# Kernel tuning notes

Measured on AMD Instinct MI355X. Metric: run time of the kernel, lower is better.

The kernel has to match this reference:

```python
import jax, jax.numpy as jnp
import numpy as np

N = 50000          # nodes
E_RAND = 800000    # random edges (avg degree 16)
IN, HID, HEADS, OUT = 256, 64, 4, 40
NEG_SLOPE = 0.2    # PyG GATConv default leaky_relu slope
BN_EPS = 1e-5


def setup_inputs() -> dict:
    key = jax.random.key(0)
    ks = jax.random.split(key, 24)
    x = jax.random.normal(ks[0], (N, IN), jnp.float32)
    ei = jax.random.randint(ks[1], (2, E_RAND), 0, N)
    loops = jnp.arange(N, dtype=ei.dtype)
    edge_index = jnp.concatenate([ei, jnp.stack([loops, loops])], axis=1)  # add self loops (PyG default)
    s = 0.1
    d = {
        "x": x,
        "edge_index": edge_index,
        "W0": jax.random.normal(ks[2], (IN, HEADS * HID), jnp.float32) * s,
        "a_src0": jax.random.normal(ks[3], (HEADS, HID), jnp.float32) * s,
        "a_dst0": jax.random.normal(ks[4], (HEADS, HID), jnp.float32) * s,
        "b0": jax.random.normal(ks[5], (HEADS * HID,), jnp.float32) * s,
        "bn0_g": jnp.ones((HEADS * HID,), jnp.float32),
        "bn0_b": jnp.zeros((HEADS * HID,), jnp.float32),
        "bn0_m": jax.random.normal(ks[6], (HEADS * HID,), jnp.float32) * s,
        "bn0_v": jax.random.uniform(ks[7], (HEADS * HID,), jnp.float32, 0.5, 1.5),
        "W1": jax.random.normal(ks[8], (HEADS * HID, HEADS * HID), jnp.float32) * s,
        "a_src1": jax.random.normal(ks[9], (HEADS, HID), jnp.float32) * s,
        "a_dst1": jax.random.normal(ks[10], (HEADS, HID), jnp.float32) * s,
        "b1": jax.random.normal(ks[11], (HEADS * HID,), jnp.float32) * s,
        "bn1_g": jnp.ones((HEADS * HID,), jnp.float32),
        "bn1_b": jnp.zeros((HEADS * HID,), jnp.float32),
        "bn1_m": jax.random.normal(ks[12], (HEADS * HID,), jnp.float32) * s,
        "bn1_v": jax.random.uniform(ks[13], (HEADS * HID,), jnp.float32, 0.5, 1.5),
        "W2": jax.random.normal(ks[14], (HEADS * HID, OUT), jnp.float32) * s,
        "a_src2": jax.random.normal(ks[15], (1, OUT), jnp.float32) * s,
        "a_dst2": jax.random.normal(ks[16], (1, OUT), jnp.float32) * s,
        "b2": jax.random.normal(ks[17], (OUT,), jnp.float32) * s,
    }
    return d


def gat_conv(x, edge_index, W, att_src, att_dst, heads, ch):
    """PyG GATConv (eval mode): gather -> leaky_relu attn -> segment softmax -> scatter add."""
    src, dst = edge_index[0], edge_index[1]
    h = (x @ W).reshape(-1, heads, ch)                       # [N,H,C]
    a_s = jnp.einsum('nhc,hc->nh', h, att_src)
    a_d = jnp.einsum('nhc,hc->nh', h, att_dst)
    e = jax.nn.leaky_relu(a_s[src] + a_d[dst], NEG_SLOPE)    # [E,H]
    m = jax.ops.segment_max(e, dst, num_segments=N)
    m = jax.lax.stop_gradient(jnp.where(jnp.isfinite(m), m, 0.0))
    p = jnp.exp(e - m[dst])
    denom = jax.ops.segment_sum(p, dst, num_segments=N)
    alpha = p / (denom[dst] + 1e-16)                         # [E,H]
    msg = h[src] * alpha[:, :, None]                         # [E,H,C]
    return jax.ops.segment_sum(msg, dst, num_segments=N)     # [N,H,C]


def _bn(h, g, b, m, v):
    return g * (h - m) * jax.lax.rsqrt(v + BN_EPS) + b


def reference(x, edge_index, W0, a_src0, a_dst0, b0, bn0_g, bn0_b, bn0_m, bn0_v,
              W1, a_src1, a_dst1, b1, bn1_g, bn1_b, bn1_m, bn1_v,
              W2, a_src2, a_dst2, b2):
    h = gat_conv(x, edge_index, W0, a_src0, a_dst0, HEADS, HID).reshape(N, HEADS * HID) + b0
    h = jax.nn.elu(_bn(h, bn0_g, bn0_b, bn0_m, bn0_v))
    h = gat_conv(h, edge_index, W1, a_src1, a_dst1, HEADS, HID).reshape(N, HEADS * HID) + b1
    h = jax.nn.elu(_bn(h, bn1_g, bn1_b, bn1_m, bn1_v))
    out = gat_conv(h, edge_index, W2, a_src2, a_dst2, 1, OUT).reshape(N, OUT) + b2
    return out
```

## Files before the change

### kernel.cpp

```cpp
#include <hip/hip_runtime.h>
#include <cstdint>
#include <cstddef>

constexpr int kN = 50000;
constexpr float kSlope = 0.2f;
constexpr float kBnEps = 1e-5f;

static inline int ceil_div(int a, int b) { return (a + b - 1) / b; }

typedef __attribute__((ext_vector_type(8))) _Float16 half8;
typedef __attribute__((ext_vector_type(8))) unsigned short ushortx8;
typedef __attribute__((ext_vector_type(4))) float f32x4;

__device__ inline unsigned short f2h_us(float f) {
  _Float16 h = (_Float16)f;
  return *(unsigned short*)&h;
}

__device__ inline void gload16(const void* g, void* l) {
  __builtin_amdgcn_global_load_lds((const __attribute__((address_space(1))) unsigned int*)g,
                                   (__attribute__((address_space(3))) unsigned int*)l, 16, 0, 0);
}


__global__ void k_degree(const int* __restrict__ dst, int* __restrict__ deg, int E) {
  int e = blockIdx.x * blockDim.x + threadIdx.x;
  if (e < E) atomicAdd(&deg[dst[e]], 1);
}

__global__ void k_scan1(const int* __restrict__ deg, int* __restrict__ rp,
                        int* __restrict__ bsum, int n) {
  __shared__ int sm[256];
  int i = blockIdx.x * 256 + threadIdx.x;
  int v = (i < n) ? deg[i] : 0;
  sm[threadIdx.x] = v;
  __syncthreads();
  for (int off = 1; off < 256; off <<= 1) {
    int t = (threadIdx.x >= off) ? sm[threadIdx.x - off] : 0;
    __syncthreads();
    sm[threadIdx.x] += t;
    __syncthreads();
  }
  if (i < n) rp[i + 1] = sm[threadIdx.x];
  if (threadIdx.x == 255) bsum[blockIdx.x] = sm[255];
}

__global__ void k_scan2(int* bsum, int nb) {
  __shared__ int sm[256];
  int v = (threadIdx.x < nb) ? bsum[threadIdx.x] : 0;
  sm[threadIdx.x] = v;
  __syncthreads();
  for (int off = 1; off < 256; off <<= 1) {
    int t = (threadIdx.x >= off) ? sm[threadIdx.x - off] : 0;
    __syncthreads();
    sm[threadIdx.x] += t;
    __syncthreads();
  }
  if (threadIdx.x < nb) bsum[threadIdx.x] = sm[threadIdx.x] - v;
}

__global__ void k_scan3(int* __restrict__ rp, const int* __restrict__ bsum, int n) {
  int i = blockIdx.x * 256 + threadIdx.x;
  if (i < n) rp[i + 1] += bsum[blockIdx.x];
  if (i == 0) rp[0] = 0;
}

__global__ void k_scatter(const int* __restrict__ src, const int* __restrict__ dst,
                          const int* __restrict__ rp, int* __restrict__ cur,
                          int* __restrict__ csr, int E) {
  int e = blockIdx.x * blockDim.x + threadIdx.x;
  if (e < E) {
    int d = dst[e];
    int pos = rp[d] + atomicAdd(&cur[d], 1);
    csr[pos] = src[e];
  }
}


__global__ void k_prep(const float* __restrict__ x, unsigned short* __restrict__ x16,
                       const float* __restrict__ W0, unsigned short* __restrict__ Wt0,
                       const float* __restrict__ W1, unsigned short* __restrict__ Wt1,
                       const float* __restrict__ W2, unsigned short* __restrict__ Wt2) {
  int i = blockIdx.x * blockDim.x + threadIdx.x;
  const int N4 = kN * 64;
  const int S0 = 256 * 256, S1 = 256 * 256, S2 = 128 * 256;
  if (i < N4) {
    float4 v = ((const float4*)x)[i];
    ushort4 o;
    o.x = f2h_us(v.x);
    o.y = f2h_us(v.y);
    o.z = f2h_us(v.z);
    o.w = f2h_us(v.w);
    ((ushort4*)x16)[i] = o;
  } else {
    int j = i - N4;
    if (j < S0) {
      int nc = j >> 8, k = j & 255;
      Wt0[j] = f2h_us(W0[(size_t)k * 256 + nc]);
    } else if (j < S0 + S1) {
      int t = j - S0;
      int nc = t >> 8, k = t & 255;
      Wt1[t] = f2h_us(W1[(size_t)k * 256 + nc]);
    } else if (j < S0 + S1 + S2) {
      int t = j - S0 - S1;
      int nc = t >> 8, k = t & 255;
      Wt2[t] = (nc < 40) ? f2h_us(W2[(size_t)k * 40 + nc]) : (unsigned short)0;
    }
  }
}


__global__ __launch_bounds__(256) void k_mfma_gemm(
    const unsigned short* __restrict__ A, const unsigned short* __restrict__ Bt,
    unsigned short* __restrict__ C, const float* __restrict__ asrc,
    const float* __restrict__ adst, float* __restrict__ a_s, float* __restrict__ a_d, int M,
    int K, int Nc, int ldc, int heads, int acols) {
  constexpr int BM = 128, BK = 32;
  __shared__ unsigned short As[BM * BK];
  __shared__ unsigned short Bs[BM * BK];
  int tid = threadIdx.x;
  int wave = tid >> 6, lane = tid & 63;
  int quad = lane >> 4, l16 = lane & 15;
  int wm = (wave & 1) * 64, wn = (wave >> 1) * 64;
  int bm = blockIdx.x * BM, bn = blockIdx.y * BM;
  int srow = lane >> 2;
  int spart = lane & 3;
  f32x4 acc[4][4] = {};
  for (int k0 = 0; k0 < K; k0 += BK) {
#pragma unroll
    for (int it = 0; it < 2; it++) {
      int chunk = wave * 2 + it;
      int row = chunk * 16 + srow;
      gload16(A + (size_t)(bm + row) * K + k0 + spart * 8, As + chunk * 512);
      gload16(Bt + (size_t)(bn + row) * K + k0 + spart * 8, Bs + chunk * 512);
    }
    __syncthreads();
    half8 af[4], bf[4];
#pragma unroll
    for (int i = 0; i < 4; i++) {
      af[i] = *(const half8*)(As + (wm + i * 16 + l16) * BK + quad * 8);
      bf[i] = *(const half8*)(Bs + (wn + i * 16 + l16) * BK + quad * 8);
    }
#pragma unroll
    for (int i = 0; i < 4; i++)
#pragma unroll
      for (int j = 0; j < 4; j++)
        acc[i][j] = __builtin_amdgcn_mfma_f32_16x16x32_f16(af[i], bf[j], acc[i][j], 0, 0, 0);
    __syncthreads();
  }
#pragma unroll
  for (int i = 0; i < 4; i++) {
#pragma unroll
    for (int j = 0; j < 4; j++) {
      int col = bn + wn + j * 16 + l16;
      if (col >= Nc) continue;
#pragma unroll
      for (int r = 0; r < 4; r++) {
        int row = bm + wm + i * 16 + quad * 4 + r;
        if (row < M) C[(size_t)row * ldc + col] = f2h_us(acc[i][j][r]);
      }
    }
  }
  int ghead = (bn + wn) >> 6;
  if (ghead < heads) {
    float asv[4], adv[4];
#pragma unroll
    for (int j = 0; j < 4; j++) {
      int col = bn + wn + j * 16 + l16;
      bool ok = col < acols;
      asv[j] = ok ? asrc[col] : 0.f;
      adv[j] = ok ? adst[col] : 0.f;
    }
#pragma unroll
    for (int i = 0; i < 4; i++) {
#pragma unroll
      for (int r = 0; r < 4; r++) {
        float s = acc[i][0][r] * asv[0] + acc[i][1][r] * asv[1] + acc[i][2][r] * asv[2] +
                  acc[i][3][r] * asv[3];
        float d = acc[i][0][r] * adv[0] + acc[i][1][r] * adv[1] + acc[i][2][r] * adv[2] +
                  acc[i][3][r] * adv[3];
#pragma unroll
        for (int mask = 1; mask <= 8; mask <<= 1) {
          s += __shfl_xor(s, mask, 64);
          d += __shfl_xor(d, mask, 64);
        }
        if (l16 == 0) {
          int row = bm + wm + i * 16 + quad * 4 + r;
          if (row < M) {
            a_s[row * heads + ghead] = s;
            a_d[row * heads + ghead] = d;
          }
        }
      }
    }
  }
}


__global__ __launch_bounds__(256, 8) void k_attn_agg256(
    const int* __restrict__ rp, const int* __restrict__ csr, const _Float16* __restrict__ h,
    const float* __restrict__ a_s, const float* __restrict__ a_d, const float* __restrict__ bias,
    const float* __restrict__ bg, const float* __restrict__ bb, const float* __restrict__ bm,
    const float* __restrict__ bv, unsigned short* __restrict__ out, int n_nodes) {
  int wid = (blockIdx.x * blockDim.x + threadIdx.x) >> 6;
  int lane = threadIdx.x & 63;
  if (wid >= n_nodes) return;
  int n = wid;
  int beg = rp[n], end = rp[n + 1];
  int half = lane >> 5, l32 = lane & 31;
  int head = l32 >> 3;
  int c = l32 * 8;
  float ad = a_d[n * 4 + head];
  float acc[8] = {};
  float psum = 0.f;
  int e = beg;
  for (; e + 16 <= end; e += 16) {
    int eb = e + half * 8;
    int s0 = csr[eb + 0];
    int s1 = csr[eb + 1];
    int s2 = csr[eb + 2];
    int s3 = csr[eb + 3];
    int s4 = csr[eb + 4];
    int s5 = csr[eb + 5];
    int s6 = csr[eb + 6];
    int s7 = csr[eb + 7];
    float t0 = a_s[s0 * 4 + head];
    float t1 = a_s[s1 * 4 + head];
    float t2 = a_s[s2 * 4 + head];
    float t3 = a_s[s3 * 4 + head];
    float t4 = a_s[s4 * 4 + head];
    float t5 = a_s[s5 * 4 + head];
    float t6 = a_s[s6 * 4 + head];
    float t7 = a_s[s7 * 4 + head];
    half8 v0 = *(const half8*)(h + (size_t)s0 * 256 + c);
    half8 v1 = *(const half8*)(h + (size_t)s1 * 256 + c);
    half8 v2 = *(const half8*)(h + (size_t)s2 * 256 + c);
    half8 v3 = *(const half8*)(h + (size_t)s3 * 256 + c);
    half8 v4 = *(const half8*)(h + (size_t)s4 * 256 + c);
    half8 v5 = *(const half8*)(h + (size_t)s5 * 256 + c);
    half8 v6 = *(const half8*)(h + (size_t)s6 * 256 + c);
    half8 v7 = *(const half8*)(h + (size_t)s7 * 256 + c);
    float x0 = t0 + ad, x1 = t1 + ad, x2 = t2 + ad, x3 = t3 + ad;
    float x4 = t4 + ad, x5 = t5 + ad, x6 = t6 + ad, x7 = t7 + ad;
    x0 = x0 > 0.f ? x0 : x0 * kSlope;
    x1 = x1 > 0.f ? x1 : x1 * kSlope;
    x2 = x2 > 0.f ? x2 : x2 * kSlope;
    x3 = x3 > 0.f ? x3 : x3 * kSlope;
    x4 = x4 > 0.f ? x4 : x4 * kSlope;
    x5 = x5 > 0.f ? x5 : x5 * kSlope;
    x6 = x6 > 0.f ? x6 : x6 * kSlope;
    x7 = x7 > 0.f ? x7 : x7 * kSlope;
    float p0 = __expf(x0), p1 = __expf(x1), p2 = __expf(x2), p3 = __expf(x3);
    float p4 = __expf(x4), p5 = __expf(x5), p6 = __expf(x6), p7 = __expf(x7);
    psum += ((p0 + p1) + (p2 + p3)) + ((p4 + p5) + (p6 + p7));
#pragma unroll
    for (int j = 0; j < 8; j++) {
      acc[j] += (float)v0[j] * p0 + (float)v1[j] * p1;
      acc[j] += (float)v2[j] * p2 + (float)v3[j] * p3;
      acc[j] += (float)v4[j] * p4 + (float)v5[j] * p5;
      acc[j] += (float)v6[j] * p6 + (float)v7[j] * p7;
    }
  }
  for (; e + 8 <= end; e += 8) {
    int s0 = csr[e + half];
    int s1 = csr[e + 2 + half];
    int s2 = csr[e + 4 + half];
    int s3 = csr[e + 6 + half];
    float x0 = a_s[s0 * 4 + head] + ad;
    float x1 = a_s[s1 * 4 + head] + ad;
    float x2 = a_s[s2 * 4 + head] + ad;
    float x3 = a_s[s3 * 4 + head] + ad;
    half8 v0 = *(const half8*)(h + (size_t)s0 * 256 + c);
    half8 v1 = *(const half8*)(h + (size_t)s1 * 256 + c);
    half8 v2 = *(const half8*)(h + (size_t)s2 * 256 + c);
    half8 v3 = *(const half8*)(h + (size_t)s3 * 256 + c);
    x0 = x0 > 0.f ? x0 : x0 * kSlope;
    x1 = x1 > 0.f ? x1 : x1 * kSlope;
    x2 = x2 > 0.f ? x2 : x2 * kSlope;
    x3 = x3 > 0.f ? x3 : x3 * kSlope;
    float p0 = __expf(x0), p1 = __expf(x1);
    float p2 = __expf(x2), p3 = __expf(x3);
    psum += (p0 + p1) + (p2 + p3);
#pragma unroll
    for (int j = 0; j < 8; j++) {
      acc[j] += (float)v0[j] * p0 + (float)v1[j] * p1;
      acc[j] += (float)v2[j] * p2 + (float)v3[j] * p3;
    }
  }
  for (; e + 2 <= end; e += 2) {
    int s0 = csr[e + half];
    float x0 = a_s[s0 * 4 + head] + ad;
    x0 = x0 > 0.f ? x0 : x0 * kSlope;
    float p0 = __expf(x0);
    psum += p0;
    half8 v0 = *(const half8*)(h + (size_t)s0 * 256 + c);
#pragma unroll
    for (int j = 0; j < 8; j++) acc[j] += (float)v0[j] * p0;
  }
  if (e < end && half == 0) {
    int s0 = csr[e];
    float x0 = a_s[s0 * 4 + head] + ad;
    x0 = x0 > 0.f ? x0 : x0 * kSlope;
    float p0 = __expf(x0);
    psum += p0;
    half8 v0 = *(const half8*)(h + (size_t)s0 * 256 + c);
#pragma unroll
    for (int j = 0; j < 8; j++) acc[j] += (float)v0[j] * p0;
  }
  psum += __shfl_xor(psum, 32, 64);
#pragma unroll
  for (int j = 0; j < 8; j++) acc[j] += __shfl_xor(acc[j], 32, 64);
  if (half == 0) {
    float rden = 1.f / (psum + 1e-16f);
    ushortx8 o;
#pragma unroll
    for (int j = 0; j < 8; j++) {
      float v = acc[j] * rden + bias[c + j];
      v = bg[c + j] * (v - bm[c + j]) * rsqrtf(bv[c + j] + kBnEps) + bb[c + j];
      v = v > 0.f ? v : (__expf(v) - 1.f);
      o[j] = f2h_us(v);
    }
    *(ushortx8*)(out + (size_t)n * 256 + c) = o;
  }
}


__global__ __launch_bounds__(256) void k_attn_agg40(
    const int* __restrict__ rp, const int* __restrict__ csr, const _Float16* __restrict__ h,
    const float* __restrict__ a_s, const float* __restrict__ a_d, const float* __restrict__ bias,
    float* __restrict__ out, int n_nodes) {
  int wid = (blockIdx.x * blockDim.x + threadIdx.x) >> 6;
  int lane = threadIdx.x & 63;
  if (wid >= n_nodes) return;
  int n = wid;
  int beg = rp[n], end = rp[n + 1];
  float ad = a_d[n];
  int grp = lane >> 3, l8 = lane & 7;
  int c = l8 * 8;
  float acc[8] = {};
  float psum = 0.f;
  for (int base = beg; base < end; base += 16) {
    int e0 = base + grp;
    int e1 = base + 8 + grp;
    if (e0 < end) {
      int s = csr[e0];
      float x = a_s[s] + ad;
      x = x > 0.f ? x : x * kSlope;
      float p = __expf(x);
      psum += p;
      half8 hv = *(const half8*)(h + (size_t)s * 64 + c);
#pragma unroll
      for (int j = 0; j < 8; j++) acc[j] += (float)hv[j] * p;
    }
    if (e1 < end) {
      int s = csr[e1];
      float x = a_s[s] + ad;
      x = x > 0.f ? x : x * kSlope;
      float p = __expf(x);
      psum += p;
      half8 hv = *(const half8*)(h + (size_t)s * 64 + c);
#pragma unroll
      for (int j = 0; j < 8; j++) acc[j] += (float)hv[j] * p;
    }
  }
#pragma unroll
  for (int mask = 8; mask <= 32; mask <<= 1) psum += __shfl_xor(psum, mask, 64);
#pragma unroll
  for (int j = 0; j < 8; j++) {
#pragma unroll
    for (int mask = 8; mask <= 32; mask <<= 1) acc[j] += __shfl_xor(acc[j], mask, 64);
  }
  if (lane < 5) {
    float rden = 1.f / (psum + 1e-16f);
    float4 o0, o1;
    o0.x = acc[0] * rden + bias[c + 0];
    o0.y = acc[1] * rden + bias[c + 1];
    o0.z = acc[2] * rden + bias[c + 2];
    o0.w = acc[3] * rden + bias[c + 3];
    o1.x = acc[4] * rden + bias[c + 4];
    o1.y = acc[5] * rden + bias[c + 5];
    o1.z = acc[6] * rden + bias[c + 6];
    o1.w = acc[7] * rden + bias[c + 7];
    *(float4*)(out + (size_t)n * 40 + c) = o0;
    *(float4*)(out + (size_t)n * 40 + c + 4) = o1;
  }
}


extern "C" void kernel_launch(void* const* d_in, const int* in_sizes, int n_in, void* d_out,
                              int out_size, void* d_ws, size_t ws_size, hipStream_t stream) {
  const float* x = (const float*)d_in[0];
  const int* ei = (const int*)d_in[1];
  const float* W0 = (const float*)d_in[2];
  const float* as0 = (const float*)d_in[3];
  const float* ad0 = (const float*)d_in[4];
  const float* b0 = (const float*)d_in[5];
  const float* bg0 = (const float*)d_in[6];
  const float* bb0 = (const float*)d_in[7];
  const float* bm0 = (const float*)d_in[8];
  const float* bv0 = (const float*)d_in[9];
  const float* W1 = (const float*)d_in[10];
  const float* as1 = (const float*)d_in[11];
  const float* ad1 = (const float*)d_in[12];
  const float* b1 = (const float*)d_in[13];
  const float* bg1 = (const float*)d_in[14];
  const float* bb1 = (const float*)d_in[15];
  const float* bm1 = (const float*)d_in[16];
  const float* bv1 = (const float*)d_in[17];
  const float* W2 = (const float*)d_in[18];
  const float* as2 = (const float*)d_in[19];
  const float* ad2 = (const float*)d_in[20];
  const float* b2 = (const float*)d_in[21];
  float* out = (float*)d_out;

  const int E = in_sizes[1] / 2;
  const int* srcIdx = ei;
  const int* dstIdx = ei + E;

  char* p = (char*)d_ws;
  auto alloc = [&](size_t bytes) -> void* {
    void* r = (void*)p;
    p += (bytes + 255) & ~(size_t)255;
    return r;
  };
  int* rp = (int*)alloc((kN + 1) * sizeof(int));
  int* degcur = (int*)alloc((size_t)2 * kN * sizeof(int));
  int* deg = degcur;
  int* cur = degcur + kN;
  int* bsum = (int*)alloc(256 * sizeof(int));
  int* csr = (int*)alloc((size_t)E * sizeof(int));
  float* a_s = (float*)alloc((size_t)kN * 4 * sizeof(float));
  float* a_d = (float*)alloc((size_t)kN * 4 * sizeof(float));
  unsigned short* x16 = (unsigned short*)alloc((size_t)kN * 256 * 2);
  unsigned short* h16 = (unsigned short*)alloc((size_t)kN * 256 * 2);
  unsigned short* act16 = (unsigned short*)alloc((size_t)kN * 256 * 2);
  unsigned short* Wt0 = (unsigned short*)alloc((size_t)256 * 256 * 2);
  unsigned short* Wt1 = (unsigned short*)alloc((size_t)256 * 256 * 2);
  unsigned short* Wt2 = (unsigned short*)alloc((size_t)128 * 256 * 2);

  const int eb = ceil_div(E, 256);
  const int nb = ceil_div(kN, 256);

  hipMemsetAsync(degcur, 0, (size_t)2 * kN * sizeof(int), stream);
  k_degree<<<eb, 256, 0, stream>>>(dstIdx, deg, E);
  k_scan1<<<nb, 256, 0, stream>>>(deg, rp, bsum, kN);
  k_scan2<<<1, 256, 0, stream>>>(bsum, nb);
  k_scan3<<<nb, 256, 0, stream>>>(rp, bsum, kN);
  k_scatter<<<eb, 256, 0, stream>>>(srcIdx, dstIdx, rp, cur, csr, E);

  const int prep_items = kN * 64 + 256 * 256 * 2 + 128 * 256;
  k_prep<<<ceil_div(prep_items, 256), 256, 0, stream>>>(x, x16, W0, Wt0, W1, Wt1, W2, Wt2);

  dim3 gg(ceil_div(kN, 128), 2);
  dim3 gg2(ceil_div(kN, 128), 1);
  int wpn_blocks = ceil_div(kN, 4);

  k_mfma_gemm<<<gg, 256, 0, stream>>>(x16, Wt0, h16, as0, ad0, a_s, a_d, kN, 256, 256, 256, 4,
                                      256);
  k_attn_agg256<<<wpn_blocks, 256, 0, stream>>>(rp, csr, (const _Float16*)h16, a_s, a_d, b0, bg0,
                                                bb0, bm0, bv0, act16, kN);

  k_mfma_gemm<<<gg, 256, 0, stream>>>(act16, Wt1, h16, as1, ad1, a_s, a_d, kN, 256, 256, 256, 4,
                                      256);
  k_attn_agg256<<<wpn_blocks, 256, 0, stream>>>(rp, csr, (const _Float16*)h16, a_s, a_d, b1, bg1,
                                                bb1, bm1, bv1, act16, kN);

  k_mfma_gemm<<<gg2, 256, 0, stream>>>(act16, Wt2, h16, as2, ad2, a_s, a_d, kN, 256, 40, 64, 1,
                                       40);
  k_attn_agg40<<<wpn_blocks, 256, 0, stream>>>(rp, csr, (const _Float16*)h16, a_s, a_d, b2, out,
                                               kN);
}
```

Measured before the change: 474.0 us.

## Double-buffer GEMM LDS tiles and drop 16-edge unrolled loop in aggregation

The MFMA GEMM now keeps two LDS buffers and issues the global-to-LDS loads for the next K tile before computing on the current one, so load latency overlaps with compute. The attention aggregation kernel loses its 16-edge unrolled main loop and its occupancy hint in launch_bounds. Neighbours are then handled by the 8-edge loop, which lowers register pressure at the cost of less memory-level parallelism per wave. The LDS footprint of the GEMM doubles.

```diff
diff --git a/kernel.cpp b/kernel.cpp
--- a/kernel.cpp
+++ b/kernel.cpp
@@ -116,8 +116,8 @@
     const float* __restrict__ adst, float* __restrict__ a_s, float* __restrict__ a_d, int M,
     int K, int Nc, int ldc, int heads, int acols) {
   constexpr int BM = 128, BK = 32;
-  __shared__ unsigned short As[BM * BK];
-  __shared__ unsigned short Bs[BM * BK];
+  __shared__ alignas(16) unsigned short As[2][BM * BK];
+  __shared__ alignas(16) unsigned short Bs[2][BM * BK];
   int tid = threadIdx.x;
   int wave = tid >> 6, lane = tid & 63;
   int quad = lane >> 4, l16 = lane & 15;
@@ -125,21 +125,29 @@
   int bm = blockIdx.x * BM, bn = blockIdx.y * BM;
   int srow = lane >> 2;
   int spart = lane & 3;
-  f32x4 acc[4][4] = {};
-  for (int k0 = 0; k0 < K; k0 += BK) {
+
+  auto stage = [&](int b, int k0) {
 #pragma unroll
     for (int it = 0; it < 2; it++) {
       int chunk = wave * 2 + it;
       int row = chunk * 16 + srow;
-      gload16(A + (size_t)(bm + row) * K + k0 + spart * 8, As + chunk * 512);
-      gload16(Bt + (size_t)(bn + row) * K + k0 + spart * 8, Bs + chunk * 512);
-    }
-    __syncthreads();
+      gload16(A + (size_t)(bm + row) * K + k0 + spart * 8, &As[b][chunk * 512]);
+      gload16(Bt + (size_t)(bn + row) * K + k0 + spart * 8, &Bs[b][chunk * 512]);
+    }
+  };
+
+  f32x4 acc[4][4] = {};
+  stage(0, 0);
+  __syncthreads();
+  int nt = K / BK;
+  int cur = 0;
+  for (int t = 0; t < nt; ++t) {
+    if (t + 1 < nt) stage(cur ^ 1, (t + 1) * BK);
     half8 af[4], bf[4];
 #pragma unroll
     for (int i = 0; i < 4; i++) {
-      af[i] = *(const half8*)(As + (wm + i * 16 + l16) * BK + quad * 8);
-      bf[i] = *(const half8*)(Bs + (wn + i * 16 + l16) * BK + quad * 8);
+      af[i] = *(const half8*)(&As[cur][(wm + i * 16 + l16) * BK + quad * 8]);
+      bf[i] = *(const half8*)(&Bs[cur][(wn + i * 16 + l16) * BK + quad * 8]);
     }
 #pragma unroll
     for (int i = 0; i < 4; i++)
@@ -147,6 +155,7 @@
       for (int j = 0; j < 4; j++)
         acc[i][j] = __builtin_amdgcn_mfma_f32_16x16x32_f16(af[i], bf[j], acc[i][j], 0, 0, 0);
     __syncthreads();
+    cur ^= 1;
   }
 #pragma unroll
   for (int i = 0; i < 4; i++) {
@@ -197,7 +206,7 @@
 }
 
 
-__global__ __launch_bounds__(256, 8) void k_attn_agg256(
+__global__ __launch_bounds__(256) void k_attn_agg256(
     const int* __restrict__ rp, const int* __restrict__ csr, const _Float16* __restrict__ h,
     const float* __restrict__ a_s, const float* __restrict__ a_d, const float* __restrict__ bias,
     const float* __restrict__ bg, const float* __restrict__ bb, const float* __restrict__ bm,
@@ -214,53 +223,6 @@
   float acc[8] = {};
   float psum = 0.f;
   int e = beg;
-  for (; e + 16 <= end; e += 16) {
-    int eb = e + half * 8;
-    int s0 = csr[eb + 0];
-    int s1 = csr[eb + 1];
-    int s2 = csr[eb + 2];
-    int s3 = csr[eb + 3];
-    int s4 = csr[eb + 4];
-    int s5 = csr[eb + 5];
-    int s6 = csr[eb + 6];
-    int s7 = csr[eb + 7];
-    float t0 = a_s[s0 * 4 + head];
-    float t1 = a_s[s1 * 4 + head];
-    float t2 = a_s[s2 * 4 + head];
-    float t3 = a_s[s3 * 4 + head];
-    float t4 = a_s[s4 * 4 + head];
-    float t5 = a_s[s5 * 4 + head];
-    float t6 = a_s[s6 * 4 + head];
-    float t7 = a_s[s7 * 4 + head];
-    half8 v0 = *(const half8*)(h + (size_t)s0 * 256 + c);
-    half8 v1 = *(const half8*)(h + (size_t)s1 * 256 + c);
-    half8 v2 = *(const half8*)(h + (size_t)s2 * 256 + c);
-    half8 v3 = *(const half8*)(h + (size_t)s3 * 256 + c);
-    half8 v4 = *(const half8*)(h + (size_t)s4 * 256 + c);
-    half8 v5 = *(const half8*)(h + (size_t)s5 * 256 + c);
-    half8 v6 = *(const half8*)(h + (size_t)s6 * 256 + c);
-    half8 v7 = *(const half8*)(h + (size_t)s7 * 256 + c);
-    float x0 = t0 + ad, x1 = t1 + ad, x2 = t2 + ad, x3 = t3 + ad;
-    float x4 = t4 + ad, x5 = t5 + ad, x6 = t6 + ad, x7 = t7 + ad;
-    x0 = x0 > 0.f ? x0 : x0 * kSlope;
-    x1 = x1 > 0.f ? x1 : x1 * kSlope;
-    x2 = x2 > 0.f ? x2 : x2 * kSlope;
-    x3 = x3 > 0.f ? x3 : x3 * kSlope;
-    x4 = x4 > 0.f ? x4 : x4 * kSlope;
-    x5 = x5 > 0.f ? x5 : x5 * kSlope;
-    x6 = x6 > 0.f ? x6 : x6 * kSlope;
-    x7 = x7 > 0.f ? x7 : x7 * kSlope;
-    float p0 = __expf(x0), p1 = __expf(x1), p2 = __expf(x2), p3 = __expf(x3);
-    float p4 = __expf(x4), p5 = __expf(x5), p6 = __expf(x6), p7 = __expf(x7);
-    psum += ((p0 + p1) + (p2 + p3)) + ((p4 + p5) + (p6 + p7));
-#pragma unroll
-    for (int j = 0; j < 8; j++) {
-      acc[j] += (float)v0[j] * p0 + (float)v1[j] * p1;
-      acc[j] += (float)v2[j] * p2 + (float)v3[j] * p3;
-      acc[j] += (float)v4[j] * p4 + (float)v5[j] * p5;
-      acc[j] += (float)v6[j] * p6 + (float)v7[j] * p7;
-    }
-  }
   for (; e + 8 <= end; e += 8) {
     int s0 = csr[e + half];
     int s1 = csr[e + 2 + half];
```

Result: faster. 452.3 us (-4.6%).
